# Optimization experiments

Measured on AMD Instinct MI355X. Metric: run time of the kernel, lower is better.

Reference implementation:

```python
import jax, jax.numpy as jnp
import numpy as np

N, E, B, L = 65536, 262144, 512, 1000
IN_DIM, HID, VOCAB = 74, 128, 25
CHANNELS = [HID, 96, 128, IN_DIM, HID]  # protein conv1d filter chain


def _conv1d(x, k):
    # x: [B, C_in, L], k: [C_out, C_in, 3], stride 1, padding 1 (like nn.Conv1d)
    return jax.lax.conv_general_dilated(x, k, (1,), ((1, 1),),
                                        dimension_numbers=('NCH', 'OIH', 'NCH'))


def setup_inputs() -> dict:
    key = jax.random.key(0)
    ks = jax.random.split(key, 20)

    def gl(k, shape, fan_in):
        return jax.random.normal(k, shape, jnp.float32) / np.float32(np.sqrt(fan_in))

    inp = {}
    inp['node_feats'] = jax.random.normal(ks[0], (N, IN_DIM), jnp.float32)
    # GraphConv (conv1): weight [in, hid]
    inp['W_gc'] = gl(ks[1], (IN_DIM, HID), IN_DIM)
    inp['b_gc'] = jnp.zeros((HID,), jnp.float32)
    # MLPNodeReadout: two linears (no activation between, per dgllife default)
    inp['W_ro_in'] = gl(ks[2], (HID, HID), HID)
    inp['b_ro_in'] = jnp.zeros((HID,), jnp.float32)
    inp['W_ro_out'] = gl(ks[3], (HID, HID), HID)
    inp['b_ro_out'] = jnp.zeros((HID,), jnp.float32)
    inp['Wc1'] = gl(ks[4], (HID, HID), HID); inp['bc1'] = jnp.zeros((HID,), jnp.float32)
    inp['Wc2'] = gl(ks[5], (HID, HID), HID); inp['bc2'] = jnp.zeros((HID,), jnp.float32)
    # protein embedding + 4 conv1d layers
    inp['embed'] = jax.random.normal(ks[6], (VOCAB, HID), jnp.float32)
    for i in range(4):
        cin, cout = CHANNELS[i], CHANNELS[i + 1]
        inp['K%d' % (i + 1)] = gl(ks[7 + i], (cout, cin, 3), cin * 3)
        inp['cb%d' % (i + 1)] = jnp.zeros((cout,), jnp.float32)
    # CPI head: Linear(2h,2h)+ReLU, Linear(2h,1)+Sigmoid
    inp['Wf1'] = gl(ks[11], (2 * HID, 2 * HID), 2 * HID); inp['bf1'] = jnp.zeros((2 * HID,), jnp.float32)
    inp['Wf2'] = gl(ks[12], (2 * HID, 1), 2 * HID); inp['bf2'] = jnp.zeros((1,), jnp.float32)
    # graph structure / protein tokens
    inp['edge_src'] = jax.random.randint(ks[13], (E,), 0, N, jnp.int32)
    inp['edge_dst'] = jax.random.randint(ks[14], (E,), 0, N, jnp.int32)
    inp['graph_ids'] = jnp.sort(jax.random.randint(ks[15], (N,), 0, B, jnp.int32))
    inp['protein_seq'] = jax.random.randint(ks[16], (B, L), 0, VOCAB, jnp.int32)
    return inp


def reference(node_feats, W_gc, b_gc, W_ro_in, b_ro_in, W_ro_out, b_ro_out,
              Wc1, bc1, Wc2, bc2, embed, K1, cb1, K2, cb2, K3, cb3, K4, cb4,
              Wf1, bf1, Wf2, bf2, edge_src, edge_dst, graph_ids, protein_seq):
    n = node_feats.shape[0]
    nb = protein_seq.shape[0]
    # dgl.add_self_loop: append self edges
    loop = jnp.arange(n, dtype=edge_src.dtype)
    src = jnp.concatenate([edge_src, loop])
    dst = jnp.concatenate([edge_dst, loop])
    ones = jnp.ones(src.shape[0], jnp.float32)
    deg_out = jax.ops.segment_sum(ones, src, n)  # out-degree (src norm)
    deg_in = jax.ops.segment_sum(ones, dst, n)   # in-degree (dst norm)
    h = node_feats * jax.lax.rsqrt(deg_out)[:, None]
    h = jax.ops.segment_sum(h[src], dst, n) * jax.lax.rsqrt(deg_in)[:, None]
    h = jax.nn.relu(h @ W_gc + b_gc)
    # MLPNodeReadout (sum over nodes per graph), then outer ReLU
    x = (h @ W_ro_in + b_ro_in) @ W_ro_out + b_ro_out
    hg = jax.nn.relu(jax.ops.segment_sum(x, graph_ids, nb))  # [B, HID]
    # compound FC layers (dropout = identity)
    cv = jax.nn.relu(hg @ Wc1 + bc1)
    cv = jax.nn.relu(cv @ Wc2 + bc2)
    pv = jnp.transpose(embed[protein_seq], (0, 2, 1))
    for K, b in ((K1, cb1), (K2, cb2), (K3, cb3), (K4, cb4)):
        pv = jax.nn.relu(_conv1d(pv, K) + b[None, :, None])
    pmax = jnp.max(pv, axis=-1)  # adaptive_max_pool1d(output_size=1) + squeeze
    # CPI head
    z = jnp.concatenate([cv, pmax], axis=1)  # [B, 2*HID]
    z = jax.nn.relu(z @ Wf1 + bf1)
    return jax.nn.sigmoid(z @ Wf2 + bf2)  # [B, 1]
```

## Files before the change

kernel.cpp:

```cpp
#include <hip/hip_runtime.h>
#include <math.h>

#define IN_DIM 74
#define HID 128
#define LSEQ 1000
#define RSA 272
#define RSB 208
#define TILE 50
#define R0 58
#define R1 56
#define R2 54
#define R3 52
#define NCHUNK 42
#define NGRP 14
#define WBUF_SZ 24576
#define LDS_BIAS 49152
#define LDS_ACT  50944
#define ACTA_SZ  15776
#define ACTB_SZ  11648
#define ACTB_BASE (LDS_ACT + 4*ACTA_SZ)
#define LDS_TOTAL (ACTB_BASE + 4*ACTB_SZ)

typedef unsigned int u32;
typedef unsigned short u16;

typedef __attribute__((ext_vector_type(8))) short bf16x8;
typedef __attribute__((ext_vector_type(4))) float f32x4;

__device__ __forceinline__ u16 f2bf(float f){
  u32 u = __float_as_uint(f);
  u32 r = (u + 0x7fffu + ((u >> 16) & 1u)) >> 16;
  return (u16)r;
}
__device__ __forceinline__ u32 pack2(float x, float y){
  return (u32)f2bf(x) | ((u32)f2bf(y) << 16);
}

__global__ void k_cnt_edge(const int* __restrict__ src, const int* __restrict__ dst,
                           int* out_cnt, int* in_cnt, int E){
  int e = blockIdx.x*256 + threadIdx.x;
  if (e < E){ atomicAdd(&out_cnt[src[e]], 1); atomicAdd(&in_cnt[dst[e]], 1); }
}
__global__ void k_scan1(const int* __restrict__ cnt, int* pref, int* bsum, int N){
  __shared__ int buf[256];
  int t = threadIdx.x, i = blockIdx.x*256 + t;
  int v = (i < N) ? cnt[i] : 0;
  buf[t] = v; __syncthreads();
  for (int o = 1; o < 256; o <<= 1){
    int tv = (t >= o) ? buf[t-o] : 0;
    __syncthreads(); buf[t] += tv; __syncthreads();
  }
  if (i < N) pref[i] = buf[t] - v;
  if (t == 255) bsum[blockIdx.x] = buf[255];
}
__global__ void k_scan2(int* bsum, int nb){
  __shared__ int buf[1024];
  int t = threadIdx.x;
  int v = (t < nb) ? bsum[t] : 0;
  buf[t] = v; __syncthreads();
  for (int o = 1; o < 1024; o <<= 1){
    int tv = (t >= o) ? buf[t-o] : 0;
    __syncthreads(); buf[t] += tv; __syncthreads();
  }
  if (t < nb) bsum[t] = buf[t] - v;
}
__global__ void k_scan3(const int* __restrict__ pref, const int* __restrict__ bsum,
                        int* offs, int* cur, int N){
  int i = blockIdx.x*256 + threadIdx.x;
  if (i < N){ int o = pref[i] + bsum[blockIdx.x]; offs[i] = o; cur[i] = o; }
}
__global__ void k_csr_fill(const int* __restrict__ src, const int* __restrict__ dst,
                           int* cur, int* csr_src, int E){
  int e = blockIdx.x*256 + threadIdx.x;
  if (e < E){ int slot = atomicAdd(&cur[dst[e]], 1); csr_src[slot] = src[e]; }
}

__global__ __launch_bounds__(256) void k_mega(const float* __restrict__ nf,
    const int* __restrict__ csr_src, const int* __restrict__ offs,
    const int* __restrict__ in_cnt, const int* __restrict__ out_cnt,
    const float* __restrict__ W, const float* __restrict__ bias,
    const int* __restrict__ gid, float* __restrict__ S, int N){
  __shared__ float Wl[IN_DIM*HID];
  __shared__ float rowsT[IN_DIM][36];
  __shared__ int lgid[32];
  const int tid = threadIdx.x;
  const int base = blockIdx.x * 32;
  for (int i = tid; i < IN_DIM*HID; i += 256) Wl[i] = W[i];
  if (tid < 32) lgid[tid] = (base + tid < N) ? gid[base + tid] : 0;

  int wid = tid >> 6, lane = tid & 63;
  for (int nn = wid; nn < 32; nn += 4){
    int d = base + nn;
    float a0 = 0.f, a1 = 0.f;
    if (d < N){
      int beg = offs[d], num = in_cnt[d];
      const float* row = nf + (size_t)d*IN_DIM;
      float ws = rsqrtf((float)out_cnt[d] + 1.f);
      a0 = row[lane]*ws;
      if (lane < IN_DIM-64) a1 = row[64+lane]*ws;
      for (int j = 0; j < num; ++j){
        int s = csr_src[beg + j];
        float w = rsqrtf((float)out_cnt[s] + 1.f);
        const float* rs = nf + (size_t)s*IN_DIM;
        a0 += rs[lane]*w;
        if (lane < IN_DIM-64) a1 += rs[64+lane]*w;
      }
      float sc = rsqrtf((float)num + 1.f);
      a0 *= sc; a1 *= sc;
    }
    rowsT[lane][nn] = a0;
    if (lane < IN_DIM-64) rowsT[64+lane][nn] = a1;
  }
  __syncthreads();

  int c = tid & 127, rh = tid >> 7;
  float acc[16];
  #pragma unroll
  for (int i = 0; i < 16; ++i) acc[i] = 0.f;
  for (int k = 0; k < IN_DIM; ++k){
    float w = Wl[k*HID + c];
    const float4* rp = (const float4*)&rowsT[k][rh*16];
    float4 r0 = rp[0], r1 = rp[1], r2 = rp[2], r3 = rp[3];
    acc[0] += r0.x*w; acc[1] += r0.y*w; acc[2] += r0.z*w; acc[3] += r0.w*w;
    acc[4] += r1.x*w; acc[5] += r1.y*w; acc[6] += r1.z*w; acc[7] += r1.w*w;
    acc[8] += r2.x*w; acc[9] += r2.y*w; acc[10] += r2.z*w; acc[11] += r2.w*w;
    acc[12] += r3.x*w; acc[13] += r3.y*w; acc[14] += r3.z*w; acc[15] += r3.w*w;
  }
  float bv = bias[c];
  float run = 0.f;
  int curg = lgid[rh*16];
  #pragma unroll
  for (int i = 0; i < 16; ++i){
    int node = rh*16 + i;
    if (base + node >= N) break;
    int g = lgid[node];
    if (g != curg){
      if (run != 0.f) atomicAdd(&S[(size_t)curg*HID + c], run);
      run = 0.f; curg = g;
    }
    run += fmaxf(acc[i] + bv, 0.f);
  }
  if (run != 0.f) atomicAdd(&S[(size_t)curg*HID + c], run);
}

__global__ __launch_bounds__(128) void k_graph_tail(const float* __restrict__ S,
    const int* __restrict__ gid,
    const float* __restrict__ W_ri, const float* __restrict__ b_ri,
    const float* __restrict__ W_ro, const float* __restrict__ b_ro,
    const float* __restrict__ Wc1, const float* __restrict__ bc1,
    const float* __restrict__ Wc2, const float* __restrict__ bc2,
    float* __restrict__ z, int N){
  __shared__ float va[128], vb[128];
  __shared__ int bounds[2];
  int g = blockIdx.x, c = threadIdx.x;
  if (c < 2){
    int target = g + c, lo = 0, hi = N;
    while (lo < hi){ int mid = (lo+hi)>>1; if (gid[mid] < target) lo = mid+1; else hi = mid; }
    bounds[c] = lo;
  }
  __syncthreads();
  float cn = (float)(bounds[1] - bounds[0]);
  va[c] = S[(size_t)g*HID + c];
  __syncthreads();
  float s = 0.f;
  for (int k = 0; k < 128; ++k) s += va[k]*W_ri[k*128 + c];
  vb[c] = s + b_ri[c]*cn;
  __syncthreads();
  s = 0.f;
  for (int k = 0; k < 128; ++k) s += vb[k]*W_ro[k*128 + c];
  va[c] = fmaxf(s + b_ro[c]*cn, 0.f);
  __syncthreads();
  s = 0.f;
  for (int k = 0; k < 128; ++k) s += va[k]*Wc1[k*128 + c];
  vb[c] = fmaxf(s + bc1[c], 0.f);
  __syncthreads();
  s = 0.f;
  for (int k = 0; k < 128; ++k) s += vb[k]*Wc2[k*128 + c];
  z[(size_t)g*256 + c] = fmaxf(s + bc2[c], 0.f);
}

__global__ void k_setup(const float* __restrict__ K1, const float* __restrict__ K2,
                        const float* __restrict__ K3, const float* __restrict__ K4,
                        const float* __restrict__ cb1, const float* __restrict__ cb2,
                        const float* __restrict__ cb3, const float* __restrict__ cb4,
                        u16* __restrict__ AW, float* __restrict__ ball,
                        float* __restrict__ z, float* __restrict__ S,
                        int* __restrict__ out_cnt, int* __restrict__ in_cnt,
                        int N, int B){
  int idx = blockIdx.x*256 + threadIdx.x;
  if (idx < NCHUNK*4096){
    int g = idx >> 12, rem = idx & 4095;
    int co = rem >> 5, kk = rem & 31;
    const float* Kw; int CIN, CPAD, COUT, ksl;
    if (g < 12)      { Kw = K1; CIN = 128; CPAD = 128; COUT =  96; ksl = g; }
    else if (g < 21) { Kw = K2; CIN =  96; CPAD =  96; COUT = 128; ksl = g-12; }
    else if (g < 33) { Kw = K3; CIN =  74; CPAD = 128; COUT =  74; ksl = g-21; }
    else             { Kw = K4; CIN =  74; CPAD =  96; COUT = 128; ksl = g-33; }
    int k = ksl*32 + kk;
    int t = k / CPAD, ci = k - t*CPAD;
    float v = (co < COUT && ci < CIN) ? Kw[((size_t)co*CIN + ci)*3 + t] : 0.f;
    int sl2 = (kk >> 3) ^ ((co >> 1) & 3);
    AW[(size_t)g*4096 + co*32 + sl2*8 + (kk & 7)] = f2bf(v);
    return;
  }
  idx -= NCHUNK*4096;
  if (idx < 448){
    float v = 0.f;
    if (idx < 96) v = cb1[idx];
    else if (idx < 224) v = cb2[idx-96];
    else if (idx < 320){ int c = idx-224; v = (c < 74) ? cb3[c] : 0.f; }
    else v = cb4[idx-320];
    ball[idx] = v;
    return;
  }
  idx -= 448;
  if (idx < B*128){ z[(size_t)(idx>>7)*256 + 128 + (idx&127)] = 0.f; return; }
  idx -= B*128;
  if (idx < B*128){ S[idx] = 0.f; return; }
  idx -= B*128;
  if (idx < 2*N){
    if (idx < N) out_cnt[idx] = 0; else in_cnt[idx-N] = 0;
  }
}

__device__ __forceinline__ void stage24k(char* lds, int tid, const u16* src, int pbuf){
  const char* s = (const char*)src;
  char* d = lds + pbuf*WBUF_SZ;
  #pragma unroll
  for (int i = 0; i < 3; ++i)
    __builtin_amdgcn_global_load_lds(
      (const __attribute__((address_space(1))) unsigned*)(s + i*8192 + tid*16),
      (__attribute__((address_space(3))) unsigned*)(d + i*8192 + tid*16), 16, 0, 0);
}

template<int KS, int G0, int M, int TPC, int RS_IN, int RCAP>
__device__ __forceinline__ void conv_phases(char* lds, const char* actIn,
    const u16* __restrict__ AW, int co0, int lm, int cg, int scg, int tid,
    f32x4 (&acc)[M][4])
{
  #pragma unroll
  for (int m = 0; m < M; ++m)
    #pragma unroll
    for (int n = 0; n < 4; ++n) acc[m][n] = (f32x4){0.f,0.f,0.f,0.f};
  #pragma unroll
  for (int ks = 0; ks < KS; ++ks){
    const int g = G0 + ks;
    const char* wb = lds + ((g/3)&1)*WBUF_SZ + (g%3)*8192;
    bf16x8 Af[M];
    #pragma unroll
    for (int m = 0; m < M; ++m)
      Af[m] = *(const bf16x8*)(wb + (co0 + m*16 + lm)*64 + scg*16);
    const int tap = ks / TPC;
    const int c16 = (ks - tap*TPC)*4 + cg;
    bf16x8 Bf[4];
    #pragma unroll
    for (int n = 0; n < 4; ++n){
      int raw = n*16 + lm + tap;
      int row = raw < RCAP ? raw : RCAP;
      Bf[n] = *(const bf16x8*)(actIn + row*RS_IN + c16*16);
    }
    __builtin_amdgcn_s_setprio(1);
    #pragma unroll
    for (int m = 0; m < M; ++m)
      #pragma unroll
      for (int n = 0; n < 4; ++n)
        acc[m][n] = __builtin_amdgcn_mfma_f32_16x16x32_bf16(Af[m], Bf[n], acc[m][n], 0, 0, 0);
    __builtin_amdgcn_s_setprio(0);
    if ((g % 3) == 2 && (ks + 1 < KS)){
      __syncthreads();
      const int gn = g/3 + 2;
      if (gn < NGRP) stage24k(lds, tid, AW + (size_t)gn*12288, gn & 1);
    }
  }
}

template<int M>
__device__ __forceinline__ void epi_store(char* actOut, int RS_OUT,
    const float* lbias, int boff, int co0, int lm, int cg,
    int lbase, int nrows, f32x4 (&acc)[M][4])
{
  #pragma unroll
  for (int m = 0; m < M; ++m){
    int co = co0 + m*16 + cg*4;
    float4 bb = *(const float4*)(lbias + boff + co);
    #pragma unroll
    for (int n = 0; n < 4; ++n){
      int r1 = n*16 + lm;
      if (r1 < nrows){
        int l = lbase + r1;
        u32 lo = 0, hi = 0;
        if ((unsigned)l < (unsigned)LSEQ){
          f32x4 a = acc[m][n];
          lo = pack2(fmaxf(a[0]+bb.x, 0.f), fmaxf(a[1]+bb.y, 0.f));
          hi = pack2(fmaxf(a[2]+bb.z, 0.f), fmaxf(a[3]+bb.w, 0.f));
        }
        uint2 st; st.x = lo; st.y = hi;
        *(uint2*)(actOut + r1*RS_OUT + co*2) = st;
      }
    }
  }
}

__device__ __forceinline__ void epi_pool(const float* lbias, int boff,
    int co0, int lm, int cg, int l0, float* __restrict__ z, int b, f32x4 (&acc)[4][4])
{
  float mxv[4][4];
  #pragma unroll
  for (int m = 0; m < 4; ++m)
    #pragma unroll
    for (int j = 0; j < 4; ++j) mxv[m][j] = 0.f;
  #pragma unroll
  for (int m = 0; m < 4; ++m){
    float4 bb = *(const float4*)(lbias + boff + co0 + m*16 + cg*4);
    const float* bv = (const float*)&bb;
    #pragma unroll
    for (int n = 0; n < 4; ++n){
      int r1 = n*16 + lm;
      int l = l0 + r1;
      if (r1 < TILE && l < LSEQ){
        #pragma unroll
        for (int j = 0; j < 4; ++j)
          mxv[m][j] = fmaxf(mxv[m][j], fmaxf(acc[m][n][j] + bv[j], 0.f));
      }
    }
  }
  #pragma unroll
  for (int o = 1; o <= 8; o <<= 1)
    #pragma unroll
    for (int m = 0; m < 4; ++m)
      #pragma unroll
      for (int j = 0; j < 4; ++j)
        mxv[m][j] = fmaxf(mxv[m][j], __shfl_xor(mxv[m][j], o));
  if (lm == 0){
    float* zrow = z + (size_t)b*256 + 128;
    #pragma unroll
    for (int m = 0; m < 4; ++m)
      #pragma unroll
      for (int j = 0; j < 4; ++j)
        atomicMax((u32*)(zrow + co0 + m*16 + cg*4 + j), __float_as_uint(mxv[m][j]));
  }
}

__global__ __launch_bounds__(512, 1) void k_protein(
    const int* __restrict__ seq, const float* __restrict__ emb,
    const u16* __restrict__ AW, const float* __restrict__ ball,
    float* __restrict__ z)
{
  __shared__ __align__(16) char lds[LDS_TOTAL];
  const int tid = threadIdx.x;
  const int lane = tid & 63, wid = tid >> 6;
  const int lm = lane & 15, cg = lane >> 4;
  const int scg = cg ^ ((lm >> 1) & 3);
  const int tl = wid >> 1;
  const int h  = wid & 1;
  const int b  = blockIdx.y;
  const int l0 = (blockIdx.x*4 + tl) * TILE;

  for (int i = tid; i < 448; i += 512) ((float*)(lds + LDS_BIAS))[i] = ball[i];

  for (int idx = tid; idx < 4*R0*16; idx += 512){
    int t2 = idx / (R0*16), rem = idx - t2*(R0*16);
    int r = rem >> 4, p = rem & 15;
    int ll0 = (blockIdx.x*4 + t2) * TILE;
    int l = ll0 - 4 + r;
    uint4 st = make_uint4(0u,0u,0u,0u);
    if ((unsigned)l < (unsigned)LSEQ){
      int tok = seq[b*LSEQ + l];
      const float4* e = (const float4*)(emb + (size_t)tok*HID + p*8);
      float4 v0 = e[0], v1 = e[1];
      st.x = pack2(v0.x, v0.y); st.y = pack2(v0.z, v0.w);
      st.z = pack2(v1.x, v1.y); st.w = pack2(v1.z, v1.w);
    }
    *(uint4*)(lds + LDS_ACT + t2*ACTA_SZ + r*RSA + p*16) = st;
  }
  stage24k(lds, tid, AW, 0);
  stage24k(lds, tid, AW + 12288, 1);
  __syncthreads();

  char* actA = lds + LDS_ACT + tl*ACTA_SZ;
  char* actB = lds + ACTB_BASE + tl*ACTB_SZ;
  const float* lbias = (const float*)(lds + LDS_BIAS);

  {
    f32x4 acc[3][4];
    conv_phases<12,0,3,4,RSA,R0-1>(lds, actA, AW, h*48, lm, cg, scg, tid, acc);
    epi_store<3>(actB, RSB, lbias, 0, h*48, lm, cg, l0-3, R1, acc);
    __syncthreads();
    stage24k(lds, tid, AW + (size_t)5*12288, 5 & 1);
  }
  {
    f32x4 acc[4][4];
    conv_phases<9,12,4,3,RSB,R1-1>(lds, actB, AW, h*64, lm, cg, scg, tid, acc);
    epi_store<4>(actA, RSA, lbias, 96, h*64, lm, cg, l0-2, R2, acc);
    __syncthreads();
    stage24k(lds, tid, AW + (size_t)8*12288, 8 & 1);
  }
  {
    f32x4 acc[3][4];
    conv_phases<12,21,3,4,RSA,R2-1>(lds, actA, AW, h*48, lm, cg, scg, tid, acc);
    epi_store<3>(actB, RSB, lbias, 224, h*48, lm, cg, l0-1, R3, acc);
    __syncthreads();
    stage24k(lds, tid, AW + (size_t)12*12288, 12 & 1);
  }
  {
    f32x4 acc[4][4];
    conv_phases<9,33,4,3,RSB,R3-1>(lds, actB, AW, h*64, lm, cg, scg, tid, acc);
    epi_pool(lbias, 320, h*64, lm, cg, l0, z, b, acc);
  }
}

__global__ __launch_bounds__(256) void k_fc_head(const float* __restrict__ z,
    const float* __restrict__ Wf1, const float* __restrict__ bf1,
    const float* __restrict__ Wf2, const float* __restrict__ bf2v,
    float* __restrict__ out){
  __shared__ float za[256];
  __shared__ float red[4];
  int r = blockIdx.x, c = threadIdx.x;
  za[c] = z[(size_t)r*256 + c];
  __syncthreads();
  float s = 0.f;
  for (int k = 0; k < 256; ++k) s += za[k]*Wf1[(size_t)k*256 + c];
  s = fmaxf(s + bf1[c], 0.f);
  float p = s * Wf2[c];
  for (int o = 32; o; o >>= 1) p += __shfl_xor(p, o);
  if ((c & 63) == 0) red[c >> 6] = p;
  __syncthreads();
  if (c == 0) out[r] = 1.f/(1.f + __expf(-(red[0]+red[1]+red[2]+red[3] + bf2v[0])));
}

extern "C" void kernel_launch(void* const* d_in, const int* in_sizes, int n_in,
                              void* d_out, int out_size, void* d_ws, size_t ws_size,
                              hipStream_t stream){
  const float* nf   = (const float*)d_in[0];
  const float* W_gc = (const float*)d_in[1];
  const float* b_gc = (const float*)d_in[2];
  const float* W_ri = (const float*)d_in[3];
  const float* b_ri = (const float*)d_in[4];
  const float* W_ro = (const float*)d_in[5];
  const float* b_ro = (const float*)d_in[6];
  const float* Wc1  = (const float*)d_in[7];
  const float* bc1  = (const float*)d_in[8];
  const float* Wc2  = (const float*)d_in[9];
  const float* bc2  = (const float*)d_in[10];
  const float* emb  = (const float*)d_in[11];
  const float* K1 = (const float*)d_in[12]; const float* cb1 = (const float*)d_in[13];
  const float* K2 = (const float*)d_in[14]; const float* cb2 = (const float*)d_in[15];
  const float* K3 = (const float*)d_in[16]; const float* cb3 = (const float*)d_in[17];
  const float* K4 = (const float*)d_in[18]; const float* cb4 = (const float*)d_in[19];
  const float* Wf1 = (const float*)d_in[20]; const float* bf1 = (const float*)d_in[21];
  const float* Wf2 = (const float*)d_in[22]; const float* bf2v = (const float*)d_in[23];
  const int* esrc = (const int*)d_in[24];
  const int* edst = (const int*)d_in[25];
  const int* gids = (const int*)d_in[26];
  const int* seq  = (const int*)d_in[27];
  float* out = (float*)d_out;

  int N = in_sizes[26];
  int E = in_sizes[24];
  int B = out_size;
  int nb = (N + 255)/256;

  char* ws = (char*)d_ws;
  size_t off = 0;
  auto take = [&](size_t bytes)->char*{
    char* p = ws + off; off = (off + bytes + 255) & ~(size_t)255; return p;
  };
  float* z      = (float*)take((size_t)B*2*HID*4);
  float* S      = (float*)take((size_t)B*HID*4);
  int* out_cnt  = (int*)take((size_t)N*4);
  int* in_cnt   = (int*)take((size_t)N*4);
  int* pref     = (int*)take((size_t)N*4);
  int* offs     = (int*)take((size_t)N*4);
  int* cur      = (int*)take((size_t)N*4);
  int* bsum     = (int*)take(1024*4);
  int* csr_src  = (int*)take((size_t)E*4);
  u16* AW       = (u16*)take((size_t)NCHUNK*8192);
  float* ball   = (float*)take(448*4);

  int setup_total = NCHUNK*4096 + 448 + B*128 + B*128 + 2*N;
  k_setup<<<(setup_total+255)/256, 256, 0, stream>>>(K1, K2, K3, K4, cb1, cb2, cb3, cb4,
                                                     AW, ball, z, S, out_cnt, in_cnt, N, B);

  k_cnt_edge<<<(E+255)/256, 256, 0, stream>>>(esrc, edst, out_cnt, in_cnt, E);
  k_scan1<<<nb, 256, 0, stream>>>(in_cnt, pref, bsum, N);
  k_scan2<<<1, 1024, 0, stream>>>(bsum, nb);
  k_scan3<<<nb, 256, 0, stream>>>(pref, bsum, offs, cur, N);
  k_csr_fill<<<(E+255)/256, 256, 0, stream>>>(esrc, edst, cur, csr_src, E);
  k_mega<<<(N+31)/32, 256, 0, stream>>>(nf, csr_src, offs, in_cnt, out_cnt,
                                        W_gc, b_gc, gids, S, N);
  k_graph_tail<<<B, 128, 0, stream>>>(S, gids, W_ri, b_ri, W_ro, b_ro,
                                      Wc1, bc1, Wc2, bc2, z, N);

  dim3 pgrid(5, B);
  k_protein<<<pgrid, 512, 0, stream>>>(seq, emb, AW, ball, z);

  k_fc_head<<<B, 256, 0, stream>>>(z, Wf1, bf1, Wf2, bf2v, out);
}
```

Measured before the change: 420.7 us.

## Shrink protein conv blocks to two tiles for two blocks per CU

Restructures the fused protein conv kernel from 512-thread blocks covering four 50-position tiles to 256-thread blocks covering two 42-position tiles, with a 12xB grid and launch bounds allowing two blocks per CU. Weight staging changes from 24KB groups of three chunks to 16KB groups of two chunks, and the explicit inter-layer weight prefetches are replaced by the in-loop staging. Bias moves from LDS to direct global loads. The aim is to cut LDS use and accumulator registers so more waves overlap, at the cost of a larger halo-to-tile ratio (more redundant conv work) and more frequent barriers.

```diff
diff --git a/kernel.cpp b/kernel.cpp
--- a/kernel.cpp
+++ b/kernel.cpp
@@ -6,20 +6,19 @@
 #define LSEQ 1000
 #define RSA 272
 #define RSB 208
-#define TILE 50
-#define R0 58
-#define R1 56
-#define R2 54
-#define R3 52
+#define TILE 42
+#define R0 50
+#define R1 48
+#define R2 46
+#define R3 44
 #define NCHUNK 42
-#define NGRP 14
-#define WBUF_SZ 24576
-#define LDS_BIAS 49152
-#define LDS_ACT  50944
-#define ACTA_SZ  15776
-#define ACTB_SZ  11648
-#define ACTB_BASE (LDS_ACT + 4*ACTA_SZ)
-#define LDS_TOTAL (ACTB_BASE + 4*ACTB_SZ)
+#define NGRP 21
+#define WBUF_SZ 16384
+#define LDS_ACT  32768
+#define ACTA_SZ  13600
+#define ACTB_SZ  9984
+#define ACTB_BASE (LDS_ACT + 2*ACTA_SZ)
+#define LDS_TOTAL (ACTB_BASE + 2*ACTB_SZ)
 
 typedef unsigned int u32;
 typedef unsigned short u16;
@@ -223,38 +222,38 @@
   }
 }
 
-__device__ __forceinline__ void stage24k(char* lds, int tid, const u16* src, int pbuf){
+__device__ __forceinline__ void stage16k(char* lds, int tid, const u16* src, int pbuf){
   const char* s = (const char*)src;
   char* d = lds + pbuf*WBUF_SZ;
   #pragma unroll
-  for (int i = 0; i < 3; ++i)
+  for (int i = 0; i < 4; ++i)
     __builtin_amdgcn_global_load_lds(
-      (const __attribute__((address_space(1))) unsigned*)(s + i*8192 + tid*16),
-      (__attribute__((address_space(3))) unsigned*)(d + i*8192 + tid*16), 16, 0, 0);
+      (const __attribute__((address_space(1))) unsigned*)(s + i*4096 + tid*16),
+      (__attribute__((address_space(3))) unsigned*)(d + i*4096 + tid*16), 16, 0, 0);
 }
 
 template<int KS, int G0, int M, int TPC, int RS_IN, int RCAP>
 __device__ __forceinline__ void conv_phases(char* lds, const char* actIn,
     const u16* __restrict__ AW, int co0, int lm, int cg, int scg, int tid,
-    f32x4 (&acc)[M][4])
+    f32x4 (&acc)[M][3])
 {
   #pragma unroll
   for (int m = 0; m < M; ++m)
     #pragma unroll
-    for (int n = 0; n < 4; ++n) acc[m][n] = (f32x4){0.f,0.f,0.f,0.f};
+    for (int n = 0; n < 3; ++n) acc[m][n] = (f32x4){0.f,0.f,0.f,0.f};
   #pragma unroll
   for (int ks = 0; ks < KS; ++ks){
     const int g = G0 + ks;
-    const char* wb = lds + ((g/3)&1)*WBUF_SZ + (g%3)*8192;
+    const char* wb = lds + ((g >> 1) & 1)*WBUF_SZ + (g & 1)*8192;
     bf16x8 Af[M];
     #pragma unroll
     for (int m = 0; m < M; ++m)
       Af[m] = *(const bf16x8*)(wb + (co0 + m*16 + lm)*64 + scg*16);
     const int tap = ks / TPC;
     const int c16 = (ks - tap*TPC)*4 + cg;
-    bf16x8 Bf[4];
-    #pragma unroll
-    for (int n = 0; n < 4; ++n){
+    bf16x8 Bf[3];
+    #pragma unroll
+    for (int n = 0; n < 3; ++n){
       int raw = n*16 + lm + tap;
       int row = raw < RCAP ? raw : RCAP;
       Bf[n] = *(const bf16x8*)(actIn + row*RS_IN + c16*16);
@@ -263,28 +262,28 @@
     #pragma unroll
     for (int m = 0; m < M; ++m)
       #pragma unroll
-      for (int n = 0; n < 4; ++n)
+      for (int n = 0; n < 3; ++n)
         acc[m][n] = __builtin_amdgcn_mfma_f32_16x16x32_bf16(Af[m], Bf[n], acc[m][n], 0, 0, 0);
     __builtin_amdgcn_s_setprio(0);
-    if ((g % 3) == 2 && (ks + 1 < KS)){
+    if ((g & 1) == 1 && g < NCHUNK-1){
       __syncthreads();
-      const int gn = g/3 + 2;
-      if (gn < NGRP) stage24k(lds, tid, AW + (size_t)gn*12288, gn & 1);
+      const int gn = (g >> 1) + 2;
+      if (gn < NGRP) stage16k(lds, tid, AW + (size_t)gn*8192, gn & 1);
     }
   }
 }
 
 template<int M>
 __device__ __forceinline__ void epi_store(char* actOut, int RS_OUT,
-    const float* lbias, int boff, int co0, int lm, int cg,
-    int lbase, int nrows, f32x4 (&acc)[M][4])
+    const float* __restrict__ bias_g, int co0, int lm, int cg,
+    int lbase, int nrows, f32x4 (&acc)[M][3])
 {
   #pragma unroll
   for (int m = 0; m < M; ++m){
     int co = co0 + m*16 + cg*4;
-    float4 bb = *(const float4*)(lbias + boff + co);
-    #pragma unroll
-    for (int n = 0; n < 4; ++n){
+    float4 bb = *(const float4*)(bias_g + co);
+    #pragma unroll
+    for (int n = 0; n < 3; ++n){
       int r1 = n*16 + lm;
       if (r1 < nrows){
         int l = lbase + r1;
@@ -301,8 +300,8 @@
   }
 }
 
-__device__ __forceinline__ void epi_pool(const float* lbias, int boff,
-    int co0, int lm, int cg, int l0, float* __restrict__ z, int b, f32x4 (&acc)[4][4])
+__device__ __forceinline__ void epi_pool(const float* __restrict__ bias_g,
+    int co0, int lm, int cg, int l0, float* __restrict__ z, int b, f32x4 (&acc)[4][3])
 {
   float mxv[4][4];
   #pragma unroll
@@ -311,10 +310,10 @@
     for (int j = 0; j < 4; ++j) mxv[m][j] = 0.f;
   #pragma unroll
   for (int m = 0; m < 4; ++m){
-    float4 bb = *(const float4*)(lbias + boff + co0 + m*16 + cg*4);
+    float4 bb = *(const float4*)(bias_g + co0 + m*16 + cg*4);
     const float* bv = (const float*)&bb;
     #pragma unroll
-    for (int n = 0; n < 4; ++n){
+    for (int n = 0; n < 3; ++n){
       int r1 = n*16 + lm;
       int l = l0 + r1;
       if (r1 < TILE && l < LSEQ){
@@ -341,7 +340,7 @@
   }
 }
 
-__global__ __launch_bounds__(512, 1) void k_protein(
+__global__ __launch_bounds__(256, 2) void k_protein(
     const int* __restrict__ seq, const float* __restrict__ emb,
     const u16* __restrict__ AW, const float* __restrict__ ball,
     float* __restrict__ z)
@@ -354,14 +353,12 @@
   const int tl = wid >> 1;
   const int h  = wid & 1;
   const int b  = blockIdx.y;
-  const int l0 = (blockIdx.x*4 + tl) * TILE;
-
-  for (int i = tid; i < 448; i += 512) ((float*)(lds + LDS_BIAS))[i] = ball[i];
-
-  for (int idx = tid; idx < 4*R0*16; idx += 512){
+  const int l0 = (blockIdx.x*2 + tl) * TILE;
+
+  for (int idx = tid; idx < 2*R0*16; idx += 256){
     int t2 = idx / (R0*16), rem = idx - t2*(R0*16);
     int r = rem >> 4, p = rem & 15;
-    int ll0 = (blockIdx.x*4 + t2) * TILE;
+    int ll0 = (blockIdx.x*2 + t2) * TILE;
     int l = ll0 - 4 + r;
     uint4 st = make_uint4(0u,0u,0u,0u);
     if ((unsigned)l < (unsigned)LSEQ){
@@ -373,39 +370,35 @@
     }
     *(uint4*)(lds + LDS_ACT + t2*ACTA_SZ + r*RSA + p*16) = st;
   }
-  stage24k(lds, tid, AW, 0);
-  stage24k(lds, tid, AW + 12288, 1);
+  stage16k(lds, tid, AW, 0);
+  stage16k(lds, tid, AW + 8192, 1);
   __syncthreads();
 
   char* actA = lds + LDS_ACT + tl*ACTA_SZ;
   char* actB = lds + ACTB_BASE + tl*ACTB_SZ;
-  const float* lbias = (const float*)(lds + LDS_BIAS);
 
   {
-    f32x4 acc[3][4];
+    f32x4 acc[3][3];
     conv_phases<12,0,3,4,RSA,R0-1>(lds, actA, AW, h*48, lm, cg, scg, tid, acc);
-    epi_store<3>(actB, RSB, lbias, 0, h*48, lm, cg, l0-3, R1, acc);
+    epi_store<3>(actB, RSB, ball + 0, h*48, lm, cg, l0-3, R1, acc);
     __syncthreads();
-    stage24k(lds, tid, AW + (size_t)5*12288, 5 & 1);
   }
   {
-    f32x4 acc[4][4];
+    f32x4 acc[4][3];
     conv_phases<9,12,4,3,RSB,R1-1>(lds, actB, AW, h*64, lm, cg, scg, tid, acc);
-    epi_store<4>(actA, RSA, lbias, 96, h*64, lm, cg, l0-2, R2, acc);
+    epi_store<4>(actA, RSA, ball + 96, h*64, lm, cg, l0-2, R2, acc);
     __syncthreads();
-    stage24k(lds, tid, AW + (size_t)8*12288, 8 & 1);
   }
   {
-    f32x4 acc[3][4];
+    f32x4 acc[3][3];
     conv_phases<12,21,3,4,RSA,R2-1>(lds, actA, AW, h*48, lm, cg, scg, tid, acc);
-    epi_store<3>(actB, RSB, lbias, 224, h*48, lm, cg, l0-1, R3, acc);
+    epi_store<3>(actB, RSB, ball + 224, h*48, lm, cg, l0-1, R3, acc);
     __syncthreads();
-    stage24k(lds, tid, AW + (size_t)12*12288, 12 & 1);
   }
   {
-    f32x4 acc[4][4];
+    f32x4 acc[4][3];
     conv_phases<9,33,4,3,RSB,R3-1>(lds, actB, AW, h*64, lm, cg, scg, tid, acc);
-    epi_pool(lbias, 320, h*64, lm, cg, l0, z, b, acc);
+    epi_pool(ball + 320, h*64, lm, cg, l0, z, b, acc);
   }
 }
 
@@ -491,8 +484,8 @@
   k_graph_tail<<<B, 128, 0, stream>>>(S, gids, W_ri, b_ri, W_ro, b_ro,
                                       Wc1, bc1, Wc2, bc2, z, N);
 
-  dim3 pgrid(5, B);
-  k_protein<<<pgrid, 512, 0, stream>>>(seq, emb, AW, ball, z);
+  dim3 pgrid(12, B);
+  k_protein<<<pgrid, 256, 0, stream>>>(seq, emb, AW, ball, z);
 
   k_fc_head<<<B, 256, 0, stream>>>(z, Wf1, bf1, Wf2, bf2v, out);
 }
```

Measured after the change: 433.4 us. 3.0% more time.

## Pre-scale node features by source norm and shrink graph-conv node tile

Applied to the files above, without the earlier changes.

Adds a kernel that multiplies each node feature row by its out-degree inverse square root once, so the gather loop in the fused graph-conv kernel no longer loads out_cnt per neighbor or computes rsqrt per edge. The neighbor index is software-prefetched one iteration ahead. Nodes per block drop from 32 to 16, doubling the grid and halving per-thread accumulators. The cost is an extra kernel launch and a full N×74 float write and read of scaled features, plus the weight matrix being staged into LDS by twice as many blocks.

```diff
diff --git a/kernel.cpp b/kernel.cpp
--- a/kernel.cpp
+++ b/kernel.cpp
@@ -41,6 +41,14 @@
   int e = blockIdx.x*256 + threadIdx.x;
   if (e < E){ atomicAdd(&out_cnt[src[e]], 1); atomicAdd(&in_cnt[dst[e]], 1); }
 }
+__global__ void k_nfs(const float* __restrict__ nf, const int* __restrict__ out_cnt,
+                      float* __restrict__ nfs, int total){
+  int idx = blockIdx.x*256 + threadIdx.x;
+  if (idx < total){
+    int i = idx / IN_DIM;
+    nfs[idx] = nf[idx] * rsqrtf((float)out_cnt[i] + 1.f);
+  }
+}
 __global__ void k_scan1(const int* __restrict__ cnt, int* pref, int* bsum, int N){
   __shared__ int buf[256];
   int t = threadIdx.x, i = blockIdx.x*256 + t;
@@ -75,35 +83,35 @@
   if (e < E){ int slot = atomicAdd(&cur[dst[e]], 1); csr_src[slot] = src[e]; }
 }
 
-__global__ __launch_bounds__(256) void k_mega(const float* __restrict__ nf,
+__global__ __launch_bounds__(256) void k_mega(const float* __restrict__ nfs,
     const int* __restrict__ csr_src, const int* __restrict__ offs,
-    const int* __restrict__ in_cnt, const int* __restrict__ out_cnt,
+    const int* __restrict__ in_cnt,
     const float* __restrict__ W, const float* __restrict__ bias,
     const int* __restrict__ gid, float* __restrict__ S, int N){
   __shared__ float Wl[IN_DIM*HID];
-  __shared__ float rowsT[IN_DIM][36];
-  __shared__ int lgid[32];
+  __shared__ float rowsT[IN_DIM][20];
+  __shared__ int lgid[16];
   const int tid = threadIdx.x;
-  const int base = blockIdx.x * 32;
+  const int base = blockIdx.x * 16;
   for (int i = tid; i < IN_DIM*HID; i += 256) Wl[i] = W[i];
-  if (tid < 32) lgid[tid] = (base + tid < N) ? gid[base + tid] : 0;
+  if (tid < 16) lgid[tid] = (base + tid < N) ? gid[base + tid] : 0;
 
   int wid = tid >> 6, lane = tid & 63;
-  for (int nn = wid; nn < 32; nn += 4){
+  for (int nn = wid; nn < 16; nn += 4){
     int d = base + nn;
     float a0 = 0.f, a1 = 0.f;
     if (d < N){
       int beg = offs[d], num = in_cnt[d];
-      const float* row = nf + (size_t)d*IN_DIM;
-      float ws = rsqrtf((float)out_cnt[d] + 1.f);
-      a0 = row[lane]*ws;
-      if (lane < IN_DIM-64) a1 = row[64+lane]*ws;
+      const float* row = nfs + (size_t)d*IN_DIM;
+      a0 = row[lane];
+      if (lane < IN_DIM-64) a1 = row[64+lane];
+      int s = (num > 0) ? csr_src[beg] : 0;
       for (int j = 0; j < num; ++j){
-        int s = csr_src[beg + j];
-        float w = rsqrtf((float)out_cnt[s] + 1.f);
-        const float* rs = nf + (size_t)s*IN_DIM;
-        a0 += rs[lane]*w;
-        if (lane < IN_DIM-64) a1 += rs[64+lane]*w;
+        int snext = (j+1 < num) ? csr_src[beg+j+1] : 0;
+        const float* rs = nfs + (size_t)s*IN_DIM;
+        a0 += rs[lane];
+        if (lane < IN_DIM-64) a1 += rs[64+lane];
+        s = snext;
       }
       float sc = rsqrtf((float)num + 1.f);
       a0 *= sc; a1 *= sc;
@@ -114,24 +122,22 @@
   __syncthreads();
 
   int c = tid & 127, rh = tid >> 7;
-  float acc[16];
-  #pragma unroll
-  for (int i = 0; i < 16; ++i) acc[i] = 0.f;
+  float acc[8];
+  #pragma unroll
+  for (int i = 0; i < 8; ++i) acc[i] = 0.f;
   for (int k = 0; k < IN_DIM; ++k){
     float w = Wl[k*HID + c];
-    const float4* rp = (const float4*)&rowsT[k][rh*16];
-    float4 r0 = rp[0], r1 = rp[1], r2 = rp[2], r3 = rp[3];
+    const float4* rp = (const float4*)&rowsT[k][rh*8];
+    float4 r0 = rp[0], r1 = rp[1];
     acc[0] += r0.x*w; acc[1] += r0.y*w; acc[2] += r0.z*w; acc[3] += r0.w*w;
     acc[4] += r1.x*w; acc[5] += r1.y*w; acc[6] += r1.z*w; acc[7] += r1.w*w;
-    acc[8] += r2.x*w; acc[9] += r2.y*w; acc[10] += r2.z*w; acc[11] += r2.w*w;
-    acc[12] += r3.x*w; acc[13] += r3.y*w; acc[14] += r3.z*w; acc[15] += r3.w*w;
   }
   float bv = bias[c];
   float run = 0.f;
-  int curg = lgid[rh*16];
-  #pragma unroll
-  for (int i = 0; i < 16; ++i){
-    int node = rh*16 + i;
+  int curg = lgid[rh*8];
+  #pragma unroll
+  for (int i = 0; i < 8; ++i){
+    int node = rh*8 + i;
     if (base + node >= N) break;
     int g = lgid[node];
     if (g != curg){
@@ -476,17 +482,19 @@
   int* csr_src  = (int*)take((size_t)E*4);
   u16* AW       = (u16*)take((size_t)NCHUNK*8192);
   float* ball   = (float*)take(448*4);
+  float* nfs    = (float*)take((size_t)N*IN_DIM*4);
 
   int setup_total = NCHUNK*4096 + 448 + B*128 + B*128 + 2*N;
   k_setup<<<(setup_total+255)/256, 256, 0, stream>>>(K1, K2, K3, K4, cb1, cb2, cb3, cb4,
                                                      AW, ball, z, S, out_cnt, in_cnt, N, B);
 
   k_cnt_edge<<<(E+255)/256, 256, 0, stream>>>(esrc, edst, out_cnt, in_cnt, E);
+  k_nfs<<<((N*IN_DIM)+255)/256, 256, 0, stream>>>(nf, out_cnt, nfs, N*IN_DIM);
   k_scan1<<<nb, 256, 0, stream>>>(in_cnt, pref, bsum, N);
   k_scan2<<<1, 1024, 0, stream>>>(bsum, nb);
   k_scan3<<<nb, 256, 0, stream>>>(pref, bsum, offs, cur, N);
   k_csr_fill<<<(E+255)/256, 256, 0, stream>>>(esrc, edst, cur, csr_src, E);
-  k_mega<<<(N+31)/32, 256, 0, stream>>>(nf, csr_src, offs, in_cnt, out_cnt,
+  k_mega<<<(N+15)/16, 256, 0, stream>>>(nfs, csr_src, offs, in_cnt,
                                         W_gc, b_gc, gids, S, N);
   k_graph_tail<<<B, 128, 0, stream>>>(S, gids, W_ri, b_ri, W_ro, b_ro,
                                       Wc1, bc1, Wc2, bc2, z, N);
```

After: 788.4 us. +87.4%, slower.
